# Kernel tuning notes

Measured on AMD Instinct MI355X. Metric: run time of the kernel, lower is better.

Reference implementation:

```python
import jax, jax.numpy as jnp
import numpy as np

U, I, E = 50000, 100000, 1600000
D, H, HID, B = 64, 8, 8, 16384
ALPHA = 0.2  # leaky relu slope


def setup_inputs() -> dict:
    key = jax.random.key(0)
    ks = jax.random.split(key, 12)
    return {
        "userIdx": jax.random.randint(ks[0], (B,), 0, U),
        "itemIdx": jax.random.randint(ks[1], (B,), 0, I),
        "edge_u": jax.random.randint(ks[2], (E,), 0, U),
        "edge_i": jax.random.randint(ks[3], (E,), 0, I),
        "uEmbd": jax.random.normal(ks[4], (U, D), dtype=jnp.float32) * 0.01,
        "iEmbd": jax.random.normal(ks[5], (I, D), dtype=jnp.float32) * 0.01,
        "Wu_h": jax.random.normal(ks[6], (H, D, HID), dtype=jnp.float32) * 0.18,
        "Wi_h": jax.random.normal(ks[7], (H, D, HID), dtype=jnp.float32) * 0.18,
        "a_h": jax.random.normal(ks[8], (H, 2 * HID), dtype=jnp.float32) * 0.3,
        "Wu_out": jax.random.normal(ks[9], (H * HID, D), dtype=jnp.float32) * 0.15,
        "Wi_out": jax.random.normal(ks[10], (H * HID, D), dtype=jnp.float32) * 0.15,
        "a_out": jax.random.normal(ks[11], (2 * D,), dtype=jnp.float32) * 0.1,
    }


def _leaky(x):
    return jnp.where(x >= 0, x, ALPHA * x)


def _gat_layer(fu, fi, Wu, Wi, a, edge_u, edge_i):
    # fu:[U,in], fi:[I,in], Wu/Wi:[in,out], a:[2*out]
    u_h = fu @ Wu  # [U,out]
    i_h = fi @ Wi  # [I,out]
    out = Wu.shape[1]
    # a . cat(u_h[eu], i_h[ei]) decomposed into per-node scores then edge gather
    su = u_h @ a[:out]  # [U]
    si = i_h @ a[out:]  # [I]
    e = jnp.exp(-_leaky(su[edge_u] + si[edge_i]))  # [E]
    rowsum = jax.ops.segment_sum(e, edge_u, num_segments=U)  # [U]
    colsum = jax.ops.segment_sum(e, edge_i, num_segments=I)  # [I]
    # users aggregate items they interacted with
    agg_i = jax.ops.segment_sum(e[:, None] * i_h[edge_i], edge_u, num_segments=U)  # [U,out]
    u_p = u_h + agg_i / jnp.where(rowsum == 0, 1.0, rowsum)[:, None]
    # items aggregate users (nan from empty cols -> 0, as in original)
    agg_u = jax.ops.segment_sum(e[:, None] * u_h[edge_u], edge_i, num_segments=I)  # [I,out]
    att_u = jnp.where((colsum > 0)[:, None], agg_u / jnp.where(colsum == 0, 1.0, colsum)[:, None], 0.0)
    i_p = i_h + att_u
    return u_p, i_p


def reference(userIdx, itemIdx, edge_u, edge_i, uEmbd, iEmbd, Wu_h, Wi_h, a_h, Wu_out, Wi_out, a_out):
    # eval mode: all dropout layers are identity
    fu, fi = uEmbd, iEmbd
    head = jax.vmap(lambda Wu, Wi, a: _gat_layer(fu, fi, Wu, Wi, a, edge_u, edge_i))
    u_ps, i_ps = head(Wu_h, Wi_h, a_h)  # [H,U,HID], [H,I,HID]
    # concat=True heads: elu then concatenate along feature dim (head-major columns)
    hu = jax.nn.elu(u_ps).transpose(1, 0, 2).reshape(U, H * HID)
    hi = jax.nn.elu(i_ps).transpose(1, 0, 2).reshape(I, H * HID)
    u_p, i_p = _gat_layer(hu, hi, Wu_out, Wi_out, a_out, edge_u, edge_i)
    u_f = jax.nn.elu(u_p)  # final F.elu in SpUIGAT
    i_f = jax.nn.elu(i_p)
    return jnp.sum(u_f[userIdx] * i_f[itemIdx], axis=1)  # [B]
```

## Files before the change

kernel.cpp:

```cpp
#include <hip/hip_runtime.h>
#include <hip/hip_fp16.h>

#define U_N 50000
#define I_N 100000
#define E_N 1600000
#define B_N 16384
#define UI_N (U_N + I_N)
#define NB_U 782
#define NB_I 1563
#define NBK 586
#define CAP 16384
#define NBLD 256
#define CHUNK (E_N / NBLD)
#define COL_CAP 3300000
#define MAXACT 32768
#define FP8_SCALE 128.0f

typedef float f32x2 __attribute__((ext_vector_type(2)));

__global__ __launch_bounds__(1024) void k_build1(
    const int* __restrict__ eu, const int* __restrict__ ei,
    int* __restrict__ bcnt, int* __restrict__ ecnt, int* __restrict__ storage) {
  __shared__ int hist[NBK];
  __shared__ int pb16[NBK];
  __shared__ int gbase[NBK];
  __shared__ int loff[NBK];
  __shared__ short map16[1344];
  __shared__ int sc[1024];
  __shared__ int sorted[21504];
  int t = threadIdx.x;
  for (int b = t; b < NBK; b += 1024) { hist[b] = 0; loff[b] = 0; }
  __syncthreads();
  int e0 = blockIdx.x * CHUNK;
  int myu[7], myi[7];
#pragma unroll
  for (int k = 0; k < 7; k++) {
    myu[k] = -1;
    if (t + 1024 * k < CHUNK) {
      int e = e0 + t + 1024 * k;
      int u = eu[e], it = ei[e];
      myu[k] = u;
      myi[k] = it;
      atomicAdd(&hist[u >> 8], 1);
      atomicAdd(&hist[(U_N + it) >> 8], 1);
    }
  }
  __syncthreads();
  int ph = (t < NBK) ? ((hist[t] + 15) & ~15) : 0;
  sc[t] = ph;
  __syncthreads();
  int val = ph;
  for (int o = 1; o < 1024; o <<= 1) {
    int x = (t >= o) ? sc[t - o] : 0;
    __syncthreads();
    val += x;
    sc[t] = val;
    __syncthreads();
  }
  int total16 = sc[1023];
  if (t < NBK) {
    int myb = val - ph;
    pb16[t] = myb;
    gbase[t] = ph ? atomicAdd(&bcnt[t], ph) : 0;
    if (hist[t]) atomicAdd(&ecnt[t], hist[t]);
    for (int k = myb >> 4; k < (myb + ph) >> 4; k++) map16[k] = (short)t;
  }
  for (int j = t; j < total16; j += 1024) sorted[j] = -1;
  __syncthreads();
#pragma unroll
  for (int k = 0; k < 7; k++) {
    if (myu[k] >= 0) {
      int u = myu[k], it = myi[k];
      int k2 = U_N + it;
      int b1 = u >> 8;
      int p1 = pb16[b1] + atomicAdd(&loff[b1], 1);
      sorted[p1] = ((u & 255) << 18) | k2;
      int b2 = k2 >> 8;
      int p2 = pb16[b2] + atomicAdd(&loff[b2], 1);
      sorted[p2] = ((k2 & 255) << 18) | u;
    }
  }
  __syncthreads();
  for (int j = t; j < total16; j += 1024) {
    int b = map16[j >> 4];
    storage[(size_t)b * CAP + gbase[b] + (j - pb16[b])] = sorted[j];
  }
}

__device__ void build2_body(int b, const int* __restrict__ bcnt,
                            const int* __restrict__ ecnt,
                            const int* __restrict__ storage,
                            int* __restrict__ ptr, int* __restrict__ col,
                            int* smem) {
  int* c = smem;
  int* sc = smem + 256;
  int* pbl = smem + 512;
  int* cur = smem + 768;
  int* tot = smem + 1024;
  int* lcol = smem + 1040;
  int t = threadIdx.x;
  int pre = 0;
  for (int i = t; i < b; i += 256) pre += ecnt[i];
  sc[t] = pre;
  c[t] = 0;
  __syncthreads();
  for (int o = 128; o > 0; o >>= 1) {
    if (t < o) sc[t] += sc[t + o];
    __syncthreads();
  }
  int base = sc[0];
  __syncthreads();
  int n = bcnt[b];
  const int* s = storage + (size_t)b * CAP;
  for (int i = t; i < n; i += 256) {
    int e = s[i];
    if (e >= 0) atomicAdd(&c[e >> 18], 1);
  }
  __syncthreads();
  int deg = c[t];
  sc[t] = deg;
  __syncthreads();
  int val = deg;
  for (int o = 1; o < 256; o <<= 1) {
    int x = (t >= o) ? sc[t - o] : 0;
    __syncthreads();
    val += x;
    sc[t] = val;
    __syncthreads();
  }
  int myoff = val - deg;
  pbl[t] = myoff;
  cur[t] = 0;
  if (t == 255) tot[0] = val;
  int node = b * 256 + t;
  if (node < UI_N) ptr[node] = base + myoff;
  if (b == NBK - 1 && t == 255) ptr[UI_N] = base + val;
  __syncthreads();
  for (int i = t; i < n; i += 256) {
    int e = s[i];
    if (e >= 0) {
      int local = e >> 18;
      int pos = pbl[local] + atomicAdd(&cur[local], 1);
      lcol[pos] = e & 0x3FFFF;
    }
  }
  __syncthreads();
  int vt = tot[0];
  for (int i = t; i < vt; i += 256) col[base + i] = lcol[i];
}

__device__ __forceinline__ void flagc_body(int bid, const int* __restrict__ uIdx,
                                           const int* __restrict__ iIdx,
                                           int* __restrict__ flag, int* __restrict__ list,
                                           int* __restrict__ nm) {
  int b = bid * 256 + threadIdx.x;
  if (b < B_N) {
    int u = uIdx[b];
    if (atomicExch(&flag[u], 1) == 0) list[atomicAdd(nm, 1)] = u;
    int it = U_N + iIdx[b];
    if (atomicExch(&flag[it], 1) == 0) list[atomicAdd(nm, 1)] = it;
  }
}

__device__ __forceinline__ void mm2_body(
    int bid, const float* __restrict__ Xu32, const float* __restrict__ Xi32,
    const __half* __restrict__ X16,
    const float* __restrict__ Wu, const float* __restrict__ Wi,
    const float* __restrict__ a, int layer,
    __half* __restrict__ f16, unsigned char* __restrict__ f8,
    __half* __restrict__ s16, const int* __restrict__ flagp,
    float* Wl, float* Xs) {
  const bool isU = bid < NB_U;
  const int N = isU ? U_N : I_N;
  const int base = (isU ? bid : bid - NB_U) * 64;
  const int gofs = isU ? 0 : U_N;
  const float* W = isU ? Wu : Wi;
  const int aoff = (layer == 1) ? (isU ? 0 : 8) : (isU ? 0 : 64);
  int t = threadIdx.x;

  if (layer == 1) {
#pragma unroll
    for (int k = 0; k < 4; k++) {
      int i = t + 256 * k;
      int h = i >> 7, d = (i >> 1) & 63, half = i & 1;
      float4 v = *(const float4*)(W + h * 512 + d * 8 + half * 4);
      *(float4*)(Wl + d * 64 + h * 8 + half * 4) = v;
    }
    const float* X = isU ? Xu32 : Xi32;
#pragma unroll
    for (int k = 0; k < 4; k++) {
      int i = t + 256 * k;
      int r = i >> 4, ch = i & 15;
      int node = base + r;
      float4 v = make_float4(0.f, 0.f, 0.f, 0.f);
      if (node < N) v = *(const float4*)(X + (size_t)node * 64 + ch * 4);
      *(float4*)(Xs + r * 64 + ch * 4) = v;
    }
  } else {
#pragma unroll
    for (int k = 0; k < 4; k++) {
      int i = t + 256 * k;
      *(float4*)(Wl + i * 4) = *(const float4*)(W + i * 4);
    }
#pragma unroll
    for (int k = 0; k < 4; k++) {
      int i = t + 256 * k;
      int r = i >> 4, ch = i & 15;
      int node = base + r;
      float4 v = make_float4(0.f, 0.f, 0.f, 0.f);
      if (node < N) {
        const __half2* hp = (const __half2*)(X16 + (size_t)(gofs + node) * 64 + ch * 4);
        float2 f0 = __half22float2(hp[0]);
        float2 f1 = __half22float2(hp[1]);
        v = make_float4(f0.x, f0.y, f1.x, f1.y);
      }
      *(float4*)(Xs + r * 64 + ch * 4) = v;
    }
  }
  __syncthreads();

  const int c0 = t & 31;
  const int rb = t >> 5;
  float acc0[8], acc1[8];
#pragma unroll
  for (int k = 0; k < 8; k++) { acc0[k] = 0.f; acc1[k] = 0.f; }

  for (int d0 = 0; d0 < 64; d0 += 4) {
    float2 wA = *(float2*)(Wl + (d0 + 0) * 64 + 2 * c0);
    float2 wB = *(float2*)(Wl + (d0 + 1) * 64 + 2 * c0);
    float2 wC = *(float2*)(Wl + (d0 + 2) * 64 + 2 * c0);
    float2 wD = *(float2*)(Wl + (d0 + 3) * 64 + 2 * c0);
#pragma unroll
    for (int k = 0; k < 8; k++) {
      float4 x = *(float4*)(Xs + (rb + 8 * k) * 64 + d0);
      acc0[k] += x.x * wA.x + x.y * wB.x + x.z * wC.x + x.w * wD.x;
      acc1[k] += x.x * wA.y + x.y * wB.y + x.z * wC.y + x.w * wD.y;
    }
  }

  float av0, av1;
  if (layer == 1) {
    int h = c0 >> 2, j = 2 * (c0 & 3);
    av0 = a[h * 16 + aoff + j];
    av1 = a[h * 16 + aoff + j + 1];
  } else {
    av0 = a[aoff + 2 * c0];
    av1 = a[aoff + 2 * c0 + 1];
  }
#pragma unroll
  for (int k = 0; k < 8; k++) {
    int node = base + rb + 8 * k;
    float s = acc0[k] * av0 + acc1[k] * av1;
    s += __shfl_xor(s, 1);
    s += __shfl_xor(s, 2);
    if (layer != 1) {
      s += __shfl_xor(s, 4);
      s += __shfl_xor(s, 8);
      s += __shfl_xor(s, 16);
    }
    if (node < N) {
      int gn = gofs + node;
      if (layer == 1 || flagp[gn]) {
        float2 f;
        f.x = acc0[k];
        f.y = acc1[k];
        *(__half2*)(f16 + (size_t)gn * 64 + 2 * c0) = __float22half2_rn(f);
      }
      int pk = __builtin_amdgcn_cvt_pk_fp8_f32(acc0[k] * FP8_SCALE,
                                               acc1[k] * FP8_SCALE, 0, false);
      *(unsigned short*)(f8 + (size_t)gn * 64 + 2 * c0) = (unsigned short)pk;
      if (layer == 1) {
        if ((c0 & 3) == 0) s16[gn * 8 + (c0 >> 2)] = __float2half_rn(s);
      } else {
        if (c0 == 0) s16[gn] = __float2half_rn(s);
      }
    }
  }
}

__global__ __launch_bounds__(256) void k_fused2(
    const int* __restrict__ bcnt, const int* __restrict__ ecnt,
    const int* __restrict__ storage,
    int* __restrict__ ptr, int* __restrict__ col,
    const int* __restrict__ uIdx, const int* __restrict__ iIdx,
    int* __restrict__ flag, int* __restrict__ list, int* __restrict__ nm,
    const float* __restrict__ uEmbd, const float* __restrict__ iEmbd,
    const float* __restrict__ Wu, const float* __restrict__ Wi,
    const float* __restrict__ a, __half* __restrict__ fA,
    unsigned char* __restrict__ fA8, __half* __restrict__ s16) {
  __shared__ __align__(16) int smem_i[11296];
  int bx = blockIdx.x;
  if (bx < NBK) {
    build2_body(bx, bcnt, ecnt, storage, ptr, col, smem_i);
  } else if (bx < NBK + 64) {
    flagc_body(bx - NBK, uIdx, iIdx, flag, list, nm);
  } else {
    float* s = (float*)smem_i;
    mm2_body(bx - NBK - 64, uEmbd, iEmbd, nullptr, Wu, Wi, a, 1, fA, fA8, s16,
             nullptr, s, s + 4096);
  }
}

__global__ __launch_bounds__(256) void k_mm2(
    const __half* __restrict__ X16, const float* __restrict__ Wu,
    const float* __restrict__ Wi, const float* __restrict__ a,
    __half* __restrict__ f16, unsigned char* __restrict__ f8,
    __half* __restrict__ s2, const int* __restrict__ flag) {
  __shared__ __align__(16) float smv[8192];
  mm2_body(blockIdx.x, nullptr, nullptr, X16, Wu, Wi, a, 2, f16, f8, s2, flag,
           smv, smv + 4096);
}

template <int LAYER>
__device__ __forceinline__ void agg_body(
    const int* __restrict__ ptr, const int* __restrict__ col,
    const unsigned char* __restrict__ f8,
    const __half* __restrict__ fA,
    __half* __restrict__ fB,
    const __half* __restrict__ sc,
    const int* __restrict__ list, const int* __restrict__ nm) {
  int gid = blockIdx.x * blockDim.x + threadIdx.x;
  int wv = gid >> 6;
  int l = threadIdx.x & 63;
  int half = l >> 5;
  int idx = wv * 2 + half;
  bool act = true;
  int n;
  if (LAYER == 2) {
    act = idx < *nm;
    n = act ? list[idx] : 0;
  } else {
    n = idx;
  }
  int lh = l & 31;
  int g = lh >> 3;
  int cc = lh & 7;

  int beg = ptr[n], endA = ptr[n + 1];
  int deg = act ? (endA - beg) : 0;
  unsigned coff = ((unsigned)(beg + g)) << 2;
  const unsigned begb = (unsigned)beg << 2;
  const unsigned f8sh = (unsigned)cc << 3;
  const unsigned ssh = (LAYER == 1) ? ((unsigned)cc << 1) : 0u;
  float sself = (LAYER == 1) ? __half2float(sc[(size_t)n * 8 + cc])
                             : __half2float(sc[n]);
  f32x2 acc2[4];
#pragma unroll
  for (int k = 0; k < 4; k++) acc2[k] = (f32x2){0.f, 0.f};
  float wsum = 0.f;
  const char* colc = (const char*)col;
  const char* f8c = (const char*)f8;
  const char* scc = (const char*)sc;

  auto edge = [&](unsigned off) {
    int nb = *(const int*)(colc + off);
    unsigned so = (LAYER == 1) ? (((unsigned)nb << 4) + ssh) : ((unsigned)nb << 1);
    float x = sself + __half2float(*(const __half*)(scc + so));
    int2 r = *(const int2*)(f8c + (((unsigned)nb << 6) + f8sh));
    float w = __expf(-fmaxf(x, 0.2f * x));
    wsum += w;
    f32x2 w2 = {w, w};
    acc2[0] += w2 * __builtin_amdgcn_cvt_pk_f32_fp8((unsigned)r.x, false);
    acc2[1] += w2 * __builtin_amdgcn_cvt_pk_f32_fp8((unsigned)r.x, true);
    acc2[2] += w2 * __builtin_amdgcn_cvt_pk_f32_fp8((unsigned)r.y, false);
    acc2[3] += w2 * __builtin_amdgcn_cvt_pk_f32_fp8((unsigned)r.y, true);
  };
  auto edgem = [&](unsigned off, bool valid) {
    unsigned o = valid ? off : begb;
    int nb = *(const int*)(colc + o);
    unsigned so = (LAYER == 1) ? (((unsigned)nb << 4) + ssh) : ((unsigned)nb << 1);
    float x = sself + __half2float(*(const __half*)(scc + so));
    int2 r = *(const int2*)(f8c + (((unsigned)nb << 6) + f8sh));
    float w = valid ? __expf(-fmaxf(x, 0.2f * x)) : 0.f;
    wsum += w;
    f32x2 w2 = {w, w};
    acc2[0] += w2 * __builtin_amdgcn_cvt_pk_f32_fp8((unsigned)r.x, false);
    acc2[1] += w2 * __builtin_amdgcn_cvt_pk_f32_fp8((unsigned)r.x, true);
    acc2[2] += w2 * __builtin_amdgcn_cvt_pk_f32_fp8((unsigned)r.y, false);
    acc2[3] += w2 * __builtin_amdgcn_cvt_pk_f32_fp8((unsigned)r.y, true);
  };

  int q = deg >> 4;
  for (; q > 0; q--) {
    edge(coff);
    edge(coff + 16);
    edge(coff + 32);
    edge(coff + 48);
    coff += 64;
  }
  int rem = deg & 15;
  if (rem) {
    edgem(coff, g < rem);
    edgem(coff + 16, (4 + g) < rem);
    if (rem > 8) {
      edgem(coff + 32, (8 + g) < rem);
      edgem(coff + 48, (12 + g) < rem);
    }
  }

#pragma unroll
  for (int k = 0; k < 4; k++) {
    f32x2 t;
    t.x = __shfl_xor(acc2[k].x, 8);
    t.y = __shfl_xor(acc2[k].y, 8);
    acc2[k] += t;
    t.x = __shfl_xor(acc2[k].x, 16);
    t.y = __shfl_xor(acc2[k].y, 16);
    acc2[k] += t;
  }
  wsum += __shfl_xor(wsum, 8);
  wsum += __shfl_xor(wsum, 16);

  if (act) {
    float inv = (deg > 0) ? 1.f / (wsum * FP8_SCALE) : 0.f;
    f32x2 a2;
    if (g == 0) a2 = acc2[0];
    else if (g == 1) a2 = acc2[1];
    else if (g == 2) a2 = acc2[2];
    else a2 = acc2[3];
    size_t boff = (size_t)n * 64 + cc * 8 + 2 * g;
    float2 sf = __half22float2(*(const __half2*)(fA + boff));
    float v0 = sf.x + a2.x * inv;
    float v1 = sf.y + a2.y * inv;
    v0 = (v0 > 0.f) ? v0 : (__expf(v0) - 1.f);
    v1 = (v1 > 0.f) ? v1 : (__expf(v1) - 1.f);
    *(__half2*)(fB + boff) = __floats2half2_rn(v0, v1);
  }
}

__global__ __launch_bounds__(256) void k_aggL1(
    const int* __restrict__ ptr, const int* __restrict__ col,
    const unsigned char* __restrict__ f8, const __half* __restrict__ fA,
    __half* __restrict__ fB, const __half* __restrict__ s16) {
  agg_body<1>(ptr, col, f8, fA, fB, s16, nullptr, nullptr);
}

__global__ __launch_bounds__(256) void k_aggL2(
    const int* __restrict__ ptr, const int* __restrict__ col,
    const unsigned char* __restrict__ f8, const __half* __restrict__ fA,
    __half* __restrict__ fB, const __half* __restrict__ s2,
    const int* __restrict__ list, const int* __restrict__ nm) {
  agg_body<2>(ptr, col, f8, fA, fB, s2, list, nm);
}

__global__ void k_dot(const int* __restrict__ uIdx, const int* __restrict__ iIdx,
                      const __half* __restrict__ u_f, const __half* __restrict__ i_f,
                      float* __restrict__ out) {
  int t = threadIdx.x;
  int pair = blockIdx.x * 32 + (t >> 3);
  int cc = t & 7;
  float4 ra = *(const float4*)(u_f + (size_t)uIdx[pair] * 64 + cc * 8);
  float4 rb = *(const float4*)(i_f + (size_t)iIdx[pair] * 64 + cc * 8);
  const __half* ha = (const __half*)&ra;
  const __half* hb = (const __half*)&rb;
  float v = 0.f;
#pragma unroll
  for (int k = 0; k < 8; k++) v += (float)ha[k] * (float)hb[k];
  v += __shfl_xor(v, 1);
  v += __shfl_xor(v, 2);
  v += __shfl_xor(v, 4);
  if (cc == 0) out[pair] = v;
}

extern "C" void kernel_launch(void* const* d_in, const int* in_sizes, int n_in,
                              void* d_out, int out_size, void* d_ws, size_t ws_size,
                              hipStream_t stream) {
  const int* userIdx = (const int*)d_in[0];
  const int* itemIdx = (const int*)d_in[1];
  const int* edge_u = (const int*)d_in[2];
  const int* edge_i = (const int*)d_in[3];
  const float* uEmbd = (const float*)d_in[4];
  const float* iEmbd = (const float*)d_in[5];
  const float* Wu_h = (const float*)d_in[6];
  const float* Wi_h = (const float*)d_in[7];
  const float* a_h = (const float*)d_in[8];
  const float* Wu_out = (const float*)d_in[9];
  const float* Wi_out = (const float*)d_in[10];
  const float* a_out = (const float*)d_in[11];
  float* out = (float*)d_out;

  char* w = (char*)d_ws;
  size_t off = 0;
  auto alloc = [&](size_t bytes) -> void* {
    void* p = w + off;
    off += (bytes + 511) & ~(size_t)511;
    return p;
  };
  int* bcnt = (int*)alloc((size_t)(2 * NBK + 16 + UI_N) * 4);
  int* ecnt = bcnt + NBK;
  int* nm = bcnt + 2 * NBK;
  int* flag = bcnt + 2 * NBK + 16;
  int* ptr = (int*)alloc((size_t)(UI_N + 1) * 4);
  int* list = (int*)alloc((size_t)MAXACT * 4);
  int* col = (int*)alloc((size_t)COL_CAP * 4);
  __half* fA = (__half*)alloc((size_t)UI_N * 64 * 2);
  unsigned char* fA8 = (unsigned char*)alloc((size_t)UI_N * 64);
  __half* s16 = (__half*)alloc((size_t)UI_N * 8 * 2);
  __half* s2 = (__half*)alloc((size_t)UI_N * 2);
  size_t union_off = off;
  int* storage = (int*)alloc((size_t)NBK * CAP * 4);
  size_t end_storage = off;
  off = union_off;
  __half* fB = (__half*)alloc((size_t)UI_N * 64 * 2);
  if (off < end_storage) off = end_storage;

  hipMemsetAsync(bcnt, 0, (size_t)(2 * NBK + 16 + UI_N) * 4, stream);
  k_build1<<<NBLD, 1024, 0, stream>>>(edge_u, edge_i, bcnt, ecnt, storage);

  k_fused2<<<NBK + 64 + NB_U + NB_I, 256, 0, stream>>>(
      bcnt, ecnt, storage, ptr, col, userIdx, itemIdx, flag, list, nm,
      uEmbd, iEmbd, Wu_h, Wi_h, a_h, fA, fA8, s16);

  k_aggL1<<<UI_N * 32 / 256, 256, 0, stream>>>(ptr, col, fA8, fA, fB, s16);

  k_mm2<<<NB_U + NB_I, 256, 0, stream>>>(fB, Wu_out, Wi_out, a_out, fA, fA8, s2, flag);
  k_aggL2<<<MAXACT * 32 / 256, 256, 0, stream>>>(ptr, col, fA8, fA, fB, s2, list, nm);

  k_dot<<<B_N / 32, 256, 0, stream>>>(userIdx, itemIdx, fB, fB + (size_t)U_N * 64, out);
}
```

Baseline: 270.4 us.

## Use 16 lanes per node in aggregation with wider fp8 loads and exp2

```diff
diff --git a/kernel.cpp b/kernel.cpp
--- a/kernel.cpp
+++ b/kernel.cpp
@@ -15,6 +15,7 @@
 #define COL_CAP 3300000
 #define MAXACT 32768
 #define FP8_SCALE 128.0f
+#define LOG2E 1.44269504088896f
 
 typedef float f32x2 __attribute__((ext_vector_type(2)));
 
@@ -270,9 +271,9 @@
                                                acc1[k] * FP8_SCALE, 0, false);
       *(unsigned short*)(f8 + (size_t)gn * 64 + 2 * c0) = (unsigned short)pk;
       if (layer == 1) {
-        if ((c0 & 3) == 0) s16[gn * 8 + (c0 >> 2)] = __float2half_rn(s);
+        if ((c0 & 3) == 0) s16[gn * 8 + (c0 >> 2)] = __float2half_rn(s * LOG2E);
       } else {
-        if (c0 == 0) s16[gn] = __float2half_rn(s);
+        if (c0 == 0) s16[gn] = __float2half_rn(s * LOG2E);
       }
     }
   }
@@ -322,8 +323,8 @@
   int gid = blockIdx.x * blockDim.x + threadIdx.x;
   int wv = gid >> 6;
   int l = threadIdx.x & 63;
-  int half = l >> 5;
-  int idx = wv * 2 + half;
+  int slice = l >> 4;
+  int idx = wv * 4 + slice;
   bool act = true;
   int n;
   if (LAYER == 2) {
@@ -332,99 +333,124 @@
   } else {
     n = idx;
   }
-  int lh = l & 31;
-  int g = lh >> 3;
-  int cc = lh & 7;
+  int lh = l & 15;
+  int g = lh >> 2;
+  int cc = lh & 3;
 
   int beg = ptr[n], endA = ptr[n + 1];
   int deg = act ? (endA - beg) : 0;
   unsigned coff = ((unsigned)(beg + g)) << 2;
   const unsigned begb = (unsigned)beg << 2;
-  const unsigned f8sh = (unsigned)cc << 3;
-  const unsigned ssh = (LAYER == 1) ? ((unsigned)cc << 1) : 0u;
-  float sself = (LAYER == 1) ? __half2float(sc[(size_t)n * 8 + cc])
-                             : __half2float(sc[n]);
-  f32x2 acc2[4];
-#pragma unroll
-  for (int k = 0; k < 4; k++) acc2[k] = (f32x2){0.f, 0.f};
-  float wsum = 0.f;
+  const unsigned f8sh = (unsigned)cc << 4;
+  float s0, s1;
+  if (LAYER == 1) {
+    __half2 sh = *(const __half2*)(sc + (size_t)n * 8 + cc * 2);
+    float2 sf = __half22float2(sh);
+    s0 = sf.x;
+    s1 = sf.y;
+  } else {
+    s0 = __half2float(sc[n]);
+    s1 = s0;
+  }
+  f32x2 acc2[8];
+#pragma unroll
+  for (int k = 0; k < 8; k++) acc2[k] = (f32x2){0.f, 0.f};
+  f32x2 wsum2 = {0.f, 0.f};
   const char* colc = (const char*)col;
   const char* f8c = (const char*)f8;
   const char* scc = (const char*)sc;
 
-  auto edge = [&](unsigned off) {
+  auto body = [&](unsigned off, float gate) {
     int nb = *(const int*)(colc + off);
-    unsigned so = (LAYER == 1) ? (((unsigned)nb << 4) + ssh) : ((unsigned)nb << 1);
-    float x = sself + __half2float(*(const __half*)(scc + so));
-    int2 r = *(const int2*)(f8c + (((unsigned)nb << 6) + f8sh));
-    float w = __expf(-fmaxf(x, 0.2f * x));
-    wsum += w;
-    f32x2 w2 = {w, w};
-    acc2[0] += w2 * __builtin_amdgcn_cvt_pk_f32_fp8((unsigned)r.x, false);
-    acc2[1] += w2 * __builtin_amdgcn_cvt_pk_f32_fp8((unsigned)r.x, true);
-    acc2[2] += w2 * __builtin_amdgcn_cvt_pk_f32_fp8((unsigned)r.y, false);
-    acc2[3] += w2 * __builtin_amdgcn_cvt_pk_f32_fp8((unsigned)r.y, true);
-  };
-  auto edgem = [&](unsigned off, bool valid) {
-    unsigned o = valid ? off : begb;
-    int nb = *(const int*)(colc + o);
-    unsigned so = (LAYER == 1) ? (((unsigned)nb << 4) + ssh) : ((unsigned)nb << 1);
-    float x = sself + __half2float(*(const __half*)(scc + so));
-    int2 r = *(const int2*)(f8c + (((unsigned)nb << 6) + f8sh));
-    float w = valid ? __expf(-fmaxf(x, 0.2f * x)) : 0.f;
-    wsum += w;
-    f32x2 w2 = {w, w};
-    acc2[0] += w2 * __builtin_amdgcn_cvt_pk_f32_fp8((unsigned)r.x, false);
-    acc2[1] += w2 * __builtin_amdgcn_cvt_pk_f32_fp8((unsigned)r.x, true);
-    acc2[2] += w2 * __builtin_amdgcn_cvt_pk_f32_fp8((unsigned)r.y, false);
-    acc2[3] += w2 * __builtin_amdgcn_cvt_pk_f32_fp8((unsigned)r.y, true);
+    int4 r = *(const int4*)(f8c + (((unsigned)nb << 6) + f8sh));
+    float w0, w1;
+    if (LAYER == 1) {
+      __half2 sh = *(const __half2*)(scc + (((unsigned)nb << 4) + ((unsigned)cc << 2)));
+      float2 sf = __half22float2(sh);
+      float x0 = s0 + sf.x, x1 = s1 + sf.y;
+      w0 = gate * exp2f(-fmaxf(x0, 0.2f * x0));
+      w1 = gate * exp2f(-fmaxf(x1, 0.2f * x1));
+    } else {
+      float x = s0 + __half2float(*(const __half*)(scc + ((unsigned)nb << 1)));
+      w0 = gate * exp2f(-fmaxf(x, 0.2f * x));
+      w1 = w0;
+    }
+    wsum2 += (f32x2){w0, w1};
+    f32x2 wa = {w0, w0}, wb = {w1, w1};
+    acc2[0] += wa * __builtin_amdgcn_cvt_pk_f32_fp8((unsigned)r.x, false);
+    acc2[1] += wa * __builtin_amdgcn_cvt_pk_f32_fp8((unsigned)r.x, true);
+    acc2[2] += wa * __builtin_amdgcn_cvt_pk_f32_fp8((unsigned)r.y, false);
+    acc2[3] += wa * __builtin_amdgcn_cvt_pk_f32_fp8((unsigned)r.y, true);
+    acc2[4] += wb * __builtin_amdgcn_cvt_pk_f32_fp8((unsigned)r.z, false);
+    acc2[5] += wb * __builtin_amdgcn_cvt_pk_f32_fp8((unsigned)r.z, true);
+    acc2[6] += wb * __builtin_amdgcn_cvt_pk_f32_fp8((unsigned)r.w, false);
+    acc2[7] += wb * __builtin_amdgcn_cvt_pk_f32_fp8((unsigned)r.w, true);
   };
 
   int q = deg >> 4;
   for (; q > 0; q--) {
-    edge(coff);
-    edge(coff + 16);
-    edge(coff + 32);
-    edge(coff + 48);
+    body(coff, 1.f);
+    body(coff + 16, 1.f);
+    body(coff + 32, 1.f);
+    body(coff + 48, 1.f);
     coff += 64;
   }
   int rem = deg & 15;
   if (rem) {
-    edgem(coff, g < rem);
-    edgem(coff + 16, (4 + g) < rem);
+    body(g < rem ? coff : begb, g < rem ? 1.f : 0.f);
+    body((4 + g) < rem ? coff + 16 : begb, (4 + g) < rem ? 1.f : 0.f);
     if (rem > 8) {
-      edgem(coff + 32, (8 + g) < rem);
-      edgem(coff + 48, (12 + g) < rem);
-    }
-  }
-
-#pragma unroll
-  for (int k = 0; k < 4; k++) {
+      body((8 + g) < rem ? coff + 32 : begb, (8 + g) < rem ? 1.f : 0.f);
+      body((12 + g) < rem ? coff + 48 : begb, (12 + g) < rem ? 1.f : 0.f);
+    }
+  }
+
+#pragma unroll
+  for (int k = 0; k < 8; k++) {
     f32x2 t;
+    t.x = __shfl_xor(acc2[k].x, 4);
+    t.y = __shfl_xor(acc2[k].y, 4);
+    acc2[k] += t;
     t.x = __shfl_xor(acc2[k].x, 8);
     t.y = __shfl_xor(acc2[k].y, 8);
     acc2[k] += t;
-    t.x = __shfl_xor(acc2[k].x, 16);
-    t.y = __shfl_xor(acc2[k].y, 16);
-    acc2[k] += t;
-  }
-  wsum += __shfl_xor(wsum, 8);
-  wsum += __shfl_xor(wsum, 16);
+  }
+  {
+    f32x2 t;
+    t.x = __shfl_xor(wsum2.x, 4);
+    t.y = __shfl_xor(wsum2.y, 4);
+    wsum2 += t;
+    t.x = __shfl_xor(wsum2.x, 8);
+    t.y = __shfl_xor(wsum2.y, 8);
+    wsum2 += t;
+  }
 
   if (act) {
-    float inv = (deg > 0) ? 1.f / (wsum * FP8_SCALE) : 0.f;
-    f32x2 a2;
-    if (g == 0) a2 = acc2[0];
-    else if (g == 1) a2 = acc2[1];
-    else if (g == 2) a2 = acc2[2];
-    else a2 = acc2[3];
-    size_t boff = (size_t)n * 64 + cc * 8 + 2 * g;
-    float2 sf = __half22float2(*(const __half2*)(fA + boff));
-    float v0 = sf.x + a2.x * inv;
-    float v1 = sf.y + a2.y * inv;
+    float ws = (g < 2) ? wsum2.x : wsum2.y;
+    float inv = (deg > 0) ? 1.f / (ws * FP8_SCALE) : 0.f;
+    f32x2 pA, pB;
+    if (g == 0) { pA = acc2[0]; pB = acc2[1]; }
+    else if (g == 1) { pA = acc2[2]; pB = acc2[3]; }
+    else if (g == 2) { pA = acc2[4]; pB = acc2[5]; }
+    else { pA = acc2[6]; pB = acc2[7]; }
+    size_t boff = (size_t)n * 64 + cc * 16 + g * 4;
+    const __half2* sp = (const __half2*)(fA + boff);
+    float2 sa = __half22float2(sp[0]);
+    float2 sb = __half22float2(sp[1]);
+    float v0 = sa.x + pA.x * inv;
+    float v1 = sa.y + pA.y * inv;
+    float v2 = sb.x + pB.x * inv;
+    float v3 = sb.y + pB.y * inv;
     v0 = (v0 > 0.f) ? v0 : (__expf(v0) - 1.f);
     v1 = (v1 > 0.f) ? v1 : (__expf(v1) - 1.f);
-    *(__half2*)(fB + boff) = __floats2half2_rn(v0, v1);
+    v2 = (v2 > 0.f) ? v2 : (__expf(v2) - 1.f);
+    v3 = (v3 > 0.f) ? v3 : (__expf(v3) - 1.f);
+    __half2 o0 = __floats2half2_rn(v0, v1);
+    __half2 o1 = __floats2half2_rn(v2, v3);
+    union { int2 i2; __half2 h2[2]; } o;
+    o.h2[0] = o0;
+    o.h2[1] = o1;
+    *(int2*)(fB + boff) = o.i2;
   }
 }
 
@@ -511,10 +537,10 @@
       bcnt, ecnt, storage, ptr, col, userIdx, itemIdx, flag, list, nm,
       uEmbd, iEmbd, Wu_h, Wi_h, a_h, fA, fA8, s16);
 
-  k_aggL1<<<UI_N * 32 / 256, 256, 0, stream>>>(ptr, col, fA8, fA, fB, s16);
+  k_aggL1<<<UI_N / 16, 256, 0, stream>>>(ptr, col, fA8, fA, fB, s16);
 
   k_mm2<<<NB_U + NB_I, 256, 0, stream>>>(fB, Wu_out, Wi_out, a_out, fA, fA8, s2, flag);
-  k_aggL2<<<MAXACT * 32 / 256, 256, 0, stream>>>(ptr, col, fA8, fA, fB, s2, list, nm);
+  k_aggL2<<<MAXACT / 16, 256, 0, stream>>>(ptr, col, fA8, fA, fB, s2, list, nm);
 
   k_dot<<<B_N / 32, 256, 0, stream>>>(userIdx, itemIdx, fB, fB + (size_t)U_N * 64, out);
 }
```

Result: slower. 282.6 us (+4.5%).

## Count node degrees with global atomics in build1 and fold log2e into scores

Applied to the files above, without the earlier changes.

```diff
diff --git a/kernel.cpp b/kernel.cpp
--- a/kernel.cpp
+++ b/kernel.cpp
@@ -15,12 +15,14 @@
 #define COL_CAP 3300000
 #define MAXACT 32768
 #define FP8_SCALE 128.0f
+#define LOG2E 1.44269504088896f
 
 typedef float f32x2 __attribute__((ext_vector_type(2)));
 
 __global__ __launch_bounds__(1024) void k_build1(
     const int* __restrict__ eu, const int* __restrict__ ei,
-    int* __restrict__ bcnt, int* __restrict__ ecnt, int* __restrict__ storage) {
+    int* __restrict__ bcnt, int* __restrict__ ecnt, int* __restrict__ deg,
+    int* __restrict__ storage) {
   __shared__ int hist[NBK];
   __shared__ int pb16[NBK];
   __shared__ int gbase[NBK];
@@ -43,6 +45,8 @@
       myi[k] = it;
       atomicAdd(&hist[u >> 8], 1);
       atomicAdd(&hist[(U_N + it) >> 8], 1);
+      atomicAdd(&deg[u], 1);
+      atomicAdd(&deg[U_N + it], 1);
     }
   }
   __syncthreads();
@@ -89,20 +93,19 @@
 
 __device__ void build2_body(int b, const int* __restrict__ bcnt,
                             const int* __restrict__ ecnt,
+                            const int* __restrict__ deg,
                             const int* __restrict__ storage,
                             int* __restrict__ ptr, int* __restrict__ col,
                             int* smem) {
-  int* c = smem;
-  int* sc = smem + 256;
-  int* pbl = smem + 512;
-  int* cur = smem + 768;
-  int* tot = smem + 1024;
-  int* lcol = smem + 1040;
+  int* sc = smem;
+  int* pb = smem + 256;
+  int* cur = smem + 512;
+  int* tot = smem + 768;
+  int* lcol = smem + 784;
   int t = threadIdx.x;
   int pre = 0;
   for (int i = t; i < b; i += 256) pre += ecnt[i];
   sc[t] = pre;
-  c[t] = 0;
   __syncthreads();
   for (int o = 128; o > 0; o >>= 1) {
     if (t < o) sc[t] += sc[t + o];
@@ -110,17 +113,11 @@
   }
   int base = sc[0];
   __syncthreads();
-  int n = bcnt[b];
-  const int* s = storage + (size_t)b * CAP;
-  for (int i = t; i < n; i += 256) {
-    int e = s[i];
-    if (e >= 0) atomicAdd(&c[e >> 18], 1);
-  }
-  __syncthreads();
-  int deg = c[t];
-  sc[t] = deg;
-  __syncthreads();
-  int val = deg;
+  int node = b * 256 + t;
+  int d = (node < UI_N) ? deg[node] : 0;
+  sc[t] = d;
+  __syncthreads();
+  int val = d;
   for (int o = 1; o < 256; o <<= 1) {
     int x = (t >= o) ? sc[t - o] : 0;
     __syncthreads();
@@ -128,19 +125,20 @@
     sc[t] = val;
     __syncthreads();
   }
-  int myoff = val - deg;
-  pbl[t] = myoff;
+  int myoff = val - d;
+  pb[t] = myoff;
   cur[t] = 0;
   if (t == 255) tot[0] = val;
-  int node = b * 256 + t;
   if (node < UI_N) ptr[node] = base + myoff;
   if (b == NBK - 1 && t == 255) ptr[UI_N] = base + val;
   __syncthreads();
+  int n = bcnt[b];
+  const int* s = storage + (size_t)b * CAP;
   for (int i = t; i < n; i += 256) {
     int e = s[i];
     if (e >= 0) {
       int local = e >> 18;
-      int pos = pbl[local] + atomicAdd(&cur[local], 1);
+      int pos = pb[local] + atomicAdd(&cur[local], 1);
       lcol[pos] = e & 0x3FFFF;
     }
   }
@@ -270,9 +268,9 @@
                                                acc1[k] * FP8_SCALE, 0, false);
       *(unsigned short*)(f8 + (size_t)gn * 64 + 2 * c0) = (unsigned short)pk;
       if (layer == 1) {
-        if ((c0 & 3) == 0) s16[gn * 8 + (c0 >> 2)] = __float2half_rn(s);
+        if ((c0 & 3) == 0) s16[gn * 8 + (c0 >> 2)] = __float2half_rn(s * LOG2E);
       } else {
-        if (c0 == 0) s16[gn] = __float2half_rn(s);
+        if (c0 == 0) s16[gn] = __float2half_rn(s * LOG2E);
       }
     }
   }
@@ -280,7 +278,7 @@
 
 __global__ __launch_bounds__(256) void k_fused2(
     const int* __restrict__ bcnt, const int* __restrict__ ecnt,
-    const int* __restrict__ storage,
+    const int* __restrict__ deg, const int* __restrict__ storage,
     int* __restrict__ ptr, int* __restrict__ col,
     const int* __restrict__ uIdx, const int* __restrict__ iIdx,
     int* __restrict__ flag, int* __restrict__ list, int* __restrict__ nm,
@@ -291,7 +289,7 @@
   __shared__ __align__(16) int smem_i[11296];
   int bx = blockIdx.x;
   if (bx < NBK) {
-    build2_body(bx, bcnt, ecnt, storage, ptr, col, smem_i);
+    build2_body(bx, bcnt, ecnt, deg, storage, ptr, col, smem_i);
   } else if (bx < NBK + 64) {
     flagc_body(bx - NBK, uIdx, iIdx, flag, list, nm);
   } else {
@@ -357,7 +355,7 @@
     unsigned so = (LAYER == 1) ? (((unsigned)nb << 4) + ssh) : ((unsigned)nb << 1);
     float x = sself + __half2float(*(const __half*)(scc + so));
     int2 r = *(const int2*)(f8c + (((unsigned)nb << 6) + f8sh));
-    float w = __expf(-fmaxf(x, 0.2f * x));
+    float w = exp2f(-fmaxf(x, 0.2f * x));
     wsum += w;
     f32x2 w2 = {w, w};
     acc2[0] += w2 * __builtin_amdgcn_cvt_pk_f32_fp8((unsigned)r.x, false);
@@ -371,7 +369,7 @@
     unsigned so = (LAYER == 1) ? (((unsigned)nb << 4) + ssh) : ((unsigned)nb << 1);
     float x = sself + __half2float(*(const __half*)(scc + so));
     int2 r = *(const int2*)(f8c + (((unsigned)nb << 6) + f8sh));
-    float w = valid ? __expf(-fmaxf(x, 0.2f * x)) : 0.f;
+    float w = valid ? exp2f(-fmaxf(x, 0.2f * x)) : 0.f;
     wsum += w;
     f32x2 w2 = {w, w};
     acc2[0] += w2 * __builtin_amdgcn_cvt_pk_f32_fp8((unsigned)r.x, false);
@@ -486,10 +484,11 @@
     off += (bytes + 511) & ~(size_t)511;
     return p;
   };
-  int* bcnt = (int*)alloc((size_t)(2 * NBK + 16 + UI_N) * 4);
+  int* bcnt = (int*)alloc((size_t)(2 * NBK + 16 + 2 * UI_N) * 4);
   int* ecnt = bcnt + NBK;
   int* nm = bcnt + 2 * NBK;
   int* flag = bcnt + 2 * NBK + 16;
+  int* deg = bcnt + 2 * NBK + 16 + UI_N;
   int* ptr = (int*)alloc((size_t)(UI_N + 1) * 4);
   int* list = (int*)alloc((size_t)MAXACT * 4);
   int* col = (int*)alloc((size_t)COL_CAP * 4);
@@ -504,17 +503,17 @@
   __half* fB = (__half*)alloc((size_t)UI_N * 64 * 2);
   if (off < end_storage) off = end_storage;
 
-  hipMemsetAsync(bcnt, 0, (size_t)(2 * NBK + 16 + UI_N) * 4, stream);
-  k_build1<<<NBLD, 1024, 0, stream>>>(edge_u, edge_i, bcnt, ecnt, storage);
+  hipMemsetAsync(bcnt, 0, (size_t)(2 * NBK + 16 + 2 * UI_N) * 4, stream);
+  k_build1<<<NBLD, 1024, 0, stream>>>(edge_u, edge_i, bcnt, ecnt, deg, storage);
 
   k_fused2<<<NBK + 64 + NB_U + NB_I, 256, 0, stream>>>(
-      bcnt, ecnt, storage, ptr, col, userIdx, itemIdx, flag, list, nm,
+      bcnt, ecnt, deg, storage, ptr, col, userIdx, itemIdx, flag, list, nm,
       uEmbd, iEmbd, Wu_h, Wi_h, a_h, fA, fA8, s16);
 
-  k_aggL1<<<UI_N * 32 / 256, 256, 0, stream>>>(ptr, col, fA8, fA, fB, s16);
+  k_aggL1<<<UI_N / 8, 256, 0, stream>>>(ptr, col, fA8, fA, fB, s16);
 
   k_mm2<<<NB_U + NB_I, 256, 0, stream>>>(fB, Wu_out, Wi_out, a_out, fA, fA8, s2, flag);
-  k_aggL2<<<MAXACT * 32 / 256, 256, 0, stream>>>(ptr, col, fA8, fA, fB, s2, list, nm);
+  k_aggL2<<<MAXACT / 8, 256, 0, stream>>>(ptr, col, fA8, fA, fB, s2, list, nm);
 
   k_dot<<<B_N / 32, 256, 0, stream>>>(userIdx, itemIdx, fB, fB + (size_t)U_N * 64, out);
 }
```

After: 390.8 us. +44.5%, slower.
